# Optimization experiments

Hardware: AMD Instinct MI355X
Metric: run time of the kernel (lower is better)

Reference implementation:

```python
import jax, jax.numpy as jnp
import numpy as np

GROUP_SIZE = 128
EPS = 1e-8


def _quantize_ste(weight, scale, group_size=GROUP_SIZE):
    """Binary {-1,+1} group-scaled quantization with straight-through estimator."""
    shape = weight.shape
    flat = weight.reshape(-1)
    n = flat.shape[0]
    pad = (-n) % group_size
    if pad:
        flat = jnp.pad(flat, (0, pad))
    groups = flat.reshape(-1, group_size)              # [n_groups, g]
    s = jnp.maximum(jnp.abs(scale[: groups.shape[0]]), EPS)[:, None]
    normalized = groups / s
    smooth = jnp.tanh(normalized)
    hard = jnp.sign(normalized)
    hard = jnp.where(hard == 0, jnp.ones_like(hard), hard)
    # STE: forward value is `hard`, gradient flows through tanh
    binary_w = jax.lax.stop_gradient(hard) + smooth - jax.lax.stop_gradient(smooth)
    quantized = binary_w * s
    return quantized.reshape(-1)[:n].reshape(shape)


def setup_inputs() -> dict:
    key = jax.random.key(0)
    k1, k2, k3, k4 = jax.random.split(key, 4)
    B, S, IN, OUT = 4, 2048, 4096, 11008
    n_groups = (OUT * IN + GROUP_SIZE - 1) // GROUP_SIZE  # 352256
    x = jax.random.normal(k1, (B, S, IN), dtype=jnp.float32)
    weight = jax.random.normal(k2, (OUT, IN), dtype=jnp.float32) * 0.02
    bias = jax.random.normal(k3, (OUT,), dtype=jnp.float32) * 0.01
    scale = jax.random.uniform(k4, (n_groups,), dtype=jnp.float32, minval=0.01, maxval=1.0)
    return {"x": x, "weight": weight, "bias": bias, "scale": scale}


def reference(x, weight, bias, scale):
    w_bin = _quantize_ste(weight, scale)               # [OUT, IN]
    # F.linear: y = x @ w_bin.T + bias
    return jnp.einsum("bsi,oi->bso", x, w_bin) + bias
```

## Files before the change

kernel.cpp:

```cpp
#include <hip/hip_runtime.h>
#include <hip/hip_bf16.h>
#include <stdint.h>

#define IN_DIM   4096
#define OUT_DIM  11008
#define M_DIM    8192

typedef unsigned short u16;
typedef __bf16 bf16_t;
typedef bf16_t bf16x8 __attribute__((ext_vector_type(8)));
typedef float  f32x4  __attribute__((ext_vector_type(4)));
typedef u16    u16x8  __attribute__((ext_vector_type(8)));

static __device__ __forceinline__ u16 f2bf(float f) {
    __bf16 h = (__bf16)f;
    return __builtin_bit_cast(unsigned short, h);
}

static __device__ __forceinline__ void async_copy16(void* lds_uniform, const void* gaddr) {
    __builtin_amdgcn_global_load_lds(
        (const __attribute__((address_space(1))) uint32_t*)(uintptr_t)gaddr,
        (__attribute__((address_space(3))) uint32_t*)(uintptr_t)lds_uniform,
        16, 0, 0);
}

#define XB_BLOCKS ((M_DIM * IN_DIM / 8) / 256)
#define WB_BLOCKS ((OUT_DIM * IN_DIM / 8) / 256)

__global__ void prep_kernel(const float* __restrict__ x, const float* __restrict__ w,
                            const float* __restrict__ scale,
                            u16x8* __restrict__ xb, u16x8* __restrict__ wb) {
    if (blockIdx.x < XB_BLOCKS) {
        int i = blockIdx.x * 256 + threadIdx.x;
        const float4* p = (const float4*)x + 2 * (size_t)i;
        float4 a = p[0];
        float4 b = p[1];
        u16x8 r;
        r[0] = f2bf(a.x); r[1] = f2bf(a.y); r[2] = f2bf(a.z); r[3] = f2bf(a.w);
        r[4] = f2bf(b.x); r[5] = f2bf(b.y); r[6] = f2bf(b.z); r[7] = f2bf(b.w);
        xb[i] = r;
    } else {
        int i = (blockIdx.x - XB_BLOCKS) * 256 + threadIdx.x;
        int g = i >> 4;
        float s = fmaxf(fabsf(scale[g]), 1e-8f);
        u16 bs = f2bf(s);
        const float4* p = (const float4*)w + 2 * (size_t)i;
        float4 a = p[0];
        float4 b = p[1];
        u16x8 r;
        r[0] = bs | ((a.x < 0.f) ? 0x8000 : 0);
        r[1] = bs | ((a.y < 0.f) ? 0x8000 : 0);
        r[2] = bs | ((a.z < 0.f) ? 0x8000 : 0);
        r[3] = bs | ((a.w < 0.f) ? 0x8000 : 0);
        r[4] = bs | ((b.x < 0.f) ? 0x8000 : 0);
        r[5] = bs | ((b.y < 0.f) ? 0x8000 : 0);
        r[6] = bs | ((b.z < 0.f) ? 0x8000 : 0);
        r[7] = bs | ((b.w < 0.f) ? 0x8000 : 0);
        wb[i] = r;
    }
}


#define NPID_M (M_DIM / 128)
#define NPID_N (OUT_DIM / 128)
#define GROUP_M 16

__global__ __launch_bounds__(256) void gemm_kernel(const u16* __restrict__ A,
                                                   const u16* __restrict__ Bw,
                                                   const float* __restrict__ bias,
                                                   float* __restrict__ out) {
    __shared__ __align__(16) u16 sA[128 * 64];
    __shared__ __align__(16) u16 sB[128 * 64];

    const int pid       = blockIdx.x;
    const int per_group = GROUP_M * NPID_N;
    const int group     = pid / per_group;
    const int pin       = pid - group * per_group;
    const int pid_m     = group * GROUP_M + (pin & (GROUP_M - 1));
    const int pid_n     = pin >> 4;

    const int tid  = threadIdx.x;
    const int w    = tid >> 6;
    const int lane = tid & 63;
    const int m0   = pid_m * 128;
    const int n0   = pid_n * 128;
    const int wm   = (w & 1) * 64;
    const int wn   = (w >> 1) * 64;

    const int lrow   = lane >> 3;
    const int lcol   = lane & 7;
    const int gchunk = lcol ^ lrow;
    const u16* gA[4];
    const u16* gB[4];
    u16* lA[4];
    u16* lB[4];
#pragma unroll
    for (int t = 0; t < 4; ++t) {
        int row = w * 32 + t * 8 + lrow;
        gA[t] = A  + (size_t)(m0 + row) * IN_DIM + gchunk * 8;
        gB[t] = Bw + (size_t)(n0 + row) * IN_DIM + gchunk * 8;
        lA[t] = &sA[(w * 4 + t) * 512];
        lB[t] = &sB[(w * 4 + t) * 512];
    }

    f32x4 acc[4][4];
#pragma unroll
    for (int mt = 0; mt < 4; ++mt)
#pragma unroll
        for (int nt = 0; nt < 4; ++nt)
            acc[mt][nt] = (f32x4){0.f, 0.f, 0.f, 0.f};

    const int row16 = lane & 15;
    const int quad  = lane >> 4;

    for (int it = 0; it < IN_DIM / 64; ++it) {
#pragma unroll
        for (int t = 0; t < 4; ++t) {
            async_copy16(lA[t], gA[t]);
            async_copy16(lB[t], gB[t]);
            gA[t] += 64;
            gB[t] += 64;
        }
        __syncthreads();

#pragma unroll
        for (int ks = 0; ks < 2; ++ks) {
            const int c = ks * 4 + quad;
            bf16x8 af[4], bfr[4];
#pragma unroll
            for (int mt = 0; mt < 4; ++mt) {
                int row = wm + mt * 16 + row16;
                af[mt] = *(const bf16x8*)&sA[row * 64 + ((c ^ (row & 7)) * 8)];
            }
#pragma unroll
            for (int nt = 0; nt < 4; ++nt) {
                int row = wn + nt * 16 + row16;
                bfr[nt] = *(const bf16x8*)&sB[row * 64 + ((c ^ (row & 7)) * 8)];
            }
#pragma unroll
            for (int mt = 0; mt < 4; ++mt)
#pragma unroll
                for (int nt = 0; nt < 4; ++nt)
                    acc[mt][nt] = __builtin_amdgcn_mfma_f32_16x16x32_bf16(
                        af[mt], bfr[nt], acc[mt][nt], 0, 0, 0);
        }
        __syncthreads();
    }

#pragma unroll
    for (int nt = 0; nt < 4; ++nt) {
        int col  = n0 + wn + nt * 16 + row16;
        float bv = bias[col];
#pragma unroll
        for (int mt = 0; mt < 4; ++mt) {
            int row = m0 + wm + mt * 16 + quad * 4;
            float* po = out + (size_t)row * OUT_DIM + col;
#pragma unroll
            for (int r = 0; r < 4; ++r)
                __builtin_nontemporal_store(acc[mt][nt][r] + bv, po + (size_t)r * OUT_DIM);
        }
    }
}

__global__ void naive_kernel(const float* __restrict__ x, const float* __restrict__ wt,
                             const float* __restrict__ bias, const float* __restrict__ scale,
                             float* __restrict__ out) {
    long idx = (long)blockIdx.x * 256 + threadIdx.x;
    if (idx >= (long)M_DIM * OUT_DIM) return;
    int m = (int)(idx / OUT_DIM);
    int o = (int)(idx % OUT_DIM);
    const float* xr = x + (size_t)m * IN_DIM;
    const float* wr = wt + (size_t)o * IN_DIM;
    float acc = 0.f;
    for (int gb = 0; gb < IN_DIM / 128; ++gb) {
        float s = fmaxf(fabsf(scale[o * (IN_DIM / 128) + gb]), 1e-8f);
        float part = 0.f;
        for (int k = 0; k < 128; ++k) {
            float wv = wr[gb * 128 + k];
            part += (wv >= 0.f) ? xr[gb * 128 + k] : -xr[gb * 128 + k];
        }
        acc += part * s;
    }
    out[idx] = acc + bias[o];
}

extern "C" void kernel_launch(void* const* d_in, const int* in_sizes, int n_in,
                              void* d_out, int out_size, void* d_ws, size_t ws_size,
                              hipStream_t stream) {
    const float* x     = (const float*)d_in[0];
    const float* wt    = (const float*)d_in[1];
    const float* bias  = (const float*)d_in[2];
    const float* scale = (const float*)d_in[3];
    float* out = (float*)d_out;

    const size_t xb_bytes = (size_t)M_DIM * IN_DIM * sizeof(u16);
    const size_t wb_bytes = (size_t)OUT_DIM * IN_DIM * sizeof(u16);

    if (ws_size >= xb_bytes + wb_bytes) {
        u16* xb = (u16*)d_ws;
        u16* wb = (u16*)((char*)d_ws + xb_bytes);

        prep_kernel<<<XB_BLOCKS + WB_BLOCKS, 256, 0, stream>>>(
            x, wt, scale, (u16x8*)xb, (u16x8*)wb);

        gemm_kernel<<<NPID_M * NPID_N, 256, 0, stream>>>(xb, wb, bias, out);
    } else {
        long total = (long)M_DIM * OUT_DIM;
        int blocks = (int)((total + 255) / 256);
        naive_kernel<<<blocks, 256, 0, stream>>>(x, wt, bias, scale, out);
    }
}
```

Baseline: 1.306 ms.

## Rewrite GEMM as 256x256 double-buffered ping-pong pipeline with 8 waves

```diff
diff --git a/kernel.cpp b/kernel.cpp
--- a/kernel.cpp
+++ b/kernel.cpp
@@ -61,98 +61,144 @@
 }
 
 
-#define NPID_M (M_DIM / 128)
-#define NPID_N (OUT_DIM / 128)
-#define GROUP_M 16
-
-__global__ __launch_bounds__(256) void gemm_kernel(const u16* __restrict__ A,
-                                                   const u16* __restrict__ Bw,
-                                                   const float* __restrict__ bias,
-                                                   float* __restrict__ out) {
-    __shared__ __align__(16) u16 sA[128 * 64];
-    __shared__ __align__(16) u16 sB[128 * 64];
-
-    const int pid       = blockIdx.x;
-    const int per_group = GROUP_M * NPID_N;
-    const int group     = pid / per_group;
-    const int pin       = pid - group * per_group;
-    const int pid_m     = group * GROUP_M + (pin & (GROUP_M - 1));
-    const int pid_n     = pin >> 4;
+#define BM 256
+#define BN 256
+#define NPID_M (M_DIM / BM)
+#define NPID_N (OUT_DIM / BN)
+
+#define BAR()        __builtin_amdgcn_s_barrier()
+#define WAIT_VM(n)   asm volatile("s_waitcnt vmcnt(" #n ")" ::: "memory")
+#define WAIT_LGKM(n) asm volatile("s_waitcnt lgkmcnt(" #n ")" ::: "memory")
+#define PRIO(p)      __builtin_amdgcn_s_setprio(p)
+#define SCHEDB()     __builtin_amdgcn_sched_barrier(0)
+
+#define STG_A(b, j, kt) async_copy16(&sA[b][((j)*64 + wid*8) * 64], \
+                                     gA + (size_t)(j) * 64 * IN_DIM + ((kt) & 63) * 64)
+#define STG_B(b, j, kt) async_copy16(&sB[b][((j)*64 + wid*8) * 64], \
+                                     gB + (size_t)(j) * 64 * IN_DIM + ((kt) & 63) * 64)
+#define STAGE_A(b, h, kt) do { STG_A(b, 2*(h), kt); STG_A(b, 2*(h)+1, kt); } while (0)
+#define STAGE_B(b, h, kt) do { STG_B(b, 2*(h), kt); STG_B(b, 2*(h)+1, kt); } while (0)
+
+#define LDA(b, mh) do {                                                   \
+    _Pragma("unroll")                                                     \
+    for (int m_ = 0; m_ < 4; ++m_) {                                      \
+      const int r_ = arb + ((mh)*4 + m_) * 16;                            \
+      aF[m_][0] = *(const bf16x8*)&sA[b][r_ * 64 + sw0];                  \
+      aF[m_][1] = *(const bf16x8*)&sA[b][r_ * 64 + sw1];                  \
+    }                                                                     \
+  } while (0)
+
+#define LDB(b, nh, BF) do {                                               \
+    _Pragma("unroll")                                                     \
+    for (int n_ = 0; n_ < 2; ++n_) {                                      \
+      const int r_ = brb + ((nh)*2 + n_) * 16;                            \
+      BF[n_][0] = *(const bf16x8*)&sB[b][r_ * 64 + sw0];                  \
+      BF[n_][1] = *(const bf16x8*)&sB[b][r_ * 64 + sw1];                  \
+    }                                                                     \
+  } while (0)
+
+#define MFMA_Q(mh, BF, nh) do {                                           \
+    _Pragma("unroll")                                                     \
+    for (int ks_ = 0; ks_ < 2; ++ks_)                                     \
+      _Pragma("unroll")                                                   \
+      for (int m_ = 0; m_ < 4; ++m_)                                      \
+        _Pragma("unroll")                                                 \
+        for (int n_ = 0; n_ < 2; ++n_)                                    \
+          acc[(mh)*4 + m_][(nh)*2 + n_] =                                 \
+              __builtin_amdgcn_mfma_f32_16x16x32_bf16(                    \
+                  aF[m_][ks_], BF[n_][ks_],                               \
+                  acc[(mh)*4 + m_][(nh)*2 + n_], 0, 0, 0);                \
+  } while (0)
+
+#define PH_TOP() do { BAR(); WAIT_LGKM(0); SCHEDB(); PRIO(1); } while (0)
+#define PH_END() do { PRIO(0); BAR(); } while (0)
+
+__global__ __launch_bounds__(512, 2) void gemm_kernel(const u16* __restrict__ A,
+                                                      const u16* __restrict__ Bw,
+                                                      const float* __restrict__ bias,
+                                                      float* __restrict__ out) {
+    __shared__ __align__(16) u16 sA[2][BM * 64];
+    __shared__ __align__(16) u16 sB[2][BN * 64];
+
+    const int pid0  = blockIdx.x;
+    const int pid   = (pid0 & 7) * (NPID_M * NPID_N / 8) + (pid0 >> 3);
+    const int pid_m = pid / NPID_N;
+    const int pid_n = pid - pid_m * NPID_N;
+    const int m0 = pid_m * BM;
+    const int n0 = pid_n * BN;
 
     const int tid  = threadIdx.x;
-    const int w    = tid >> 6;
+    const int wid  = tid >> 6;
     const int lane = tid & 63;
-    const int m0   = pid_m * 128;
-    const int n0   = pid_n * 128;
-    const int wm   = (w & 1) * 64;
-    const int wn   = (w >> 1) * 64;
-
-    const int lrow   = lane >> 3;
-    const int lcol   = lane & 7;
-    const int gchunk = lcol ^ lrow;
-    const u16* gA[4];
-    const u16* gB[4];
-    u16* lA[4];
-    u16* lB[4];
-#pragma unroll
-    for (int t = 0; t < 4; ++t) {
-        int row = w * 32 + t * 8 + lrow;
-        gA[t] = A  + (size_t)(m0 + row) * IN_DIM + gchunk * 8;
-        gB[t] = Bw + (size_t)(n0 + row) * IN_DIM + gchunk * 8;
-        lA[t] = &sA[(w * 4 + t) * 512];
-        lB[t] = &sB[(w * 4 + t) * 512];
-    }
-
-    f32x4 acc[4][4];
-#pragma unroll
-    for (int mt = 0; mt < 4; ++mt)
+    const int wm   = (wid >> 2) * 128;
+    const int wn   = (wid & 3) * 64;
+
+    const int lrow = lane >> 3;
+    const int gc   = (lane & 7) ^ lrow;
+    const u16* gA = A  + (size_t)(m0 + wid * 8 + lrow) * IN_DIM + gc * 8;
+    const u16* gB = Bw + (size_t)(n0 + wid * 8 + lrow) * IN_DIM + gc * 8;
+
+    const int row16 = lane & 15;
+    const int quad  = lane >> 4;
+    const int arb   = wm + row16;
+    const int brb   = wn + row16;
+    const int sw0   = ((0 * 4 + quad) ^ (row16 & 7)) * 8;
+    const int sw1   = ((1 * 4 + quad) ^ (row16 & 7)) * 8;
+
+    f32x4 acc[8][4];
+#pragma unroll
+    for (int mt = 0; mt < 8; ++mt)
 #pragma unroll
         for (int nt = 0; nt < 4; ++nt)
             acc[mt][nt] = (f32x4){0.f, 0.f, 0.f, 0.f};
 
-    const int row16 = lane & 15;
-    const int quad  = lane >> 4;
-
-    for (int it = 0; it < IN_DIM / 64; ++it) {
-#pragma unroll
-        for (int t = 0; t < 4; ++t) {
-            async_copy16(lA[t], gA[t]);
-            async_copy16(lB[t], gB[t]);
-            gA[t] += 64;
-            gB[t] += 64;
-        }
-        __syncthreads();
-
-#pragma unroll
-        for (int ks = 0; ks < 2; ++ks) {
-            const int c = ks * 4 + quad;
-            bf16x8 af[4], bfr[4];
-#pragma unroll
-            for (int mt = 0; mt < 4; ++mt) {
-                int row = wm + mt * 16 + row16;
-                af[mt] = *(const bf16x8*)&sA[row * 64 + ((c ^ (row & 7)) * 8)];
-            }
-#pragma unroll
-            for (int nt = 0; nt < 4; ++nt) {
-                int row = wn + nt * 16 + row16;
-                bfr[nt] = *(const bf16x8*)&sB[row * 64 + ((c ^ (row & 7)) * 8)];
-            }
-#pragma unroll
-            for (int mt = 0; mt < 4; ++mt)
-#pragma unroll
-                for (int nt = 0; nt < 4; ++nt)
-                    acc[mt][nt] = __builtin_amdgcn_mfma_f32_16x16x32_bf16(
-                        af[mt], bfr[nt], acc[mt][nt], 0, 0, 0);
-        }
-        __syncthreads();
-    }
+    bf16x8 aF[4][2], bF0[2][2], bF1[2][2];
+
+    STAGE_A(0, 0, 0); STAGE_A(0, 1, 0);
+    STAGE_B(0, 0, 0); STAGE_B(0, 1, 0);
+    STAGE_B(1, 0, 1); STAGE_A(1, 0, 1);
+    WAIT_VM(4);
+    BAR();
+
+    for (int i = 0; i < IN_DIM / 128; ++i) {
+        const int kt = 2 * i;
+        LDA(0, 0); LDB(0, 0, bF0);
+        STAGE_A(1, 1, kt + 1);
+        WAIT_LGKM(8);
+        PH_TOP(); MFMA_Q(0, bF0, 0); PH_END();
+        LDB(0, 1, bF1);
+        STAGE_B(1, 1, kt + 1);
+        PH_TOP(); MFMA_Q(0, bF1, 1); PH_END();
+        LDA(0, 1);
+        STAGE_B(0, 0, kt + 2);
+        PH_TOP(); MFMA_Q(1, bF0, 0); PH_END();
+        STAGE_A(0, 0, kt + 2);
+        BAR(); WAIT_LGKM(0); SCHEDB(); PRIO(1);
+        MFMA_Q(1, bF1, 1);
+        PRIO(0); WAIT_VM(4); BAR();
+        LDA(1, 0); LDB(1, 0, bF0);
+        STAGE_A(0, 1, kt + 2);
+        WAIT_LGKM(8);
+        PH_TOP(); MFMA_Q(0, bF0, 0); PH_END();
+        LDB(1, 1, bF1);
+        STAGE_B(0, 1, kt + 2);
+        PH_TOP(); MFMA_Q(0, bF1, 1); PH_END();
+        LDA(1, 1);
+        STAGE_B(1, 0, kt + 3);
+        PH_TOP(); MFMA_Q(1, bF0, 0); PH_END();
+        STAGE_A(1, 0, kt + 3);
+        BAR(); WAIT_LGKM(0); SCHEDB(); PRIO(1);
+        MFMA_Q(1, bF1, 1);
+        PRIO(0); WAIT_VM(4); BAR();
+    }
+    WAIT_VM(0);
 
 #pragma unroll
     for (int nt = 0; nt < 4; ++nt) {
         int col  = n0 + wn + nt * 16 + row16;
         float bv = bias[col];
 #pragma unroll
-        for (int mt = 0; mt < 4; ++mt) {
+        for (int mt = 0; mt < 8; ++mt) {
             int row = m0 + wm + mt * 16 + quad * 4;
             float* po = out + (size_t)row * OUT_DIM + col;
 #pragma unroll
@@ -203,7 +249,7 @@
         prep_kernel<<<XB_BLOCKS + WB_BLOCKS, 256, 0, stream>>>(
             x, wt, scale, (u16x8*)xb, (u16x8*)wb);
 
-        gemm_kernel<<<NPID_M * NPID_N, 256, 0, stream>>>(xb, wb, bias, out);
+        gemm_kernel<<<NPID_M * NPID_N, 512, 0, stream>>>(xb, wb, bias, out);
     } else {
         long total = (long)M_DIM * OUT_DIM;
         int blocks = (int)((total + 255) / 256);
```

Result: faster. 1.136 ms (-13.1%).
